# Optimization experiments

Measured on AMD Instinct MI355X. Metric: run time of the kernel, lower is better.

## Reference

```python
import jax, jax.numpy as jnp
import numpy as np

B, S, H = 4, 2048, 512
E, K = 8, 2
DFF = 4 * H


def setup_inputs() -> dict:
    key = jax.random.key(0)
    ks = jax.random.split(key, 6)
    x = jax.random.normal(ks[0], (B, S, H), dtype=jnp.float32)
    gate_W = jax.random.normal(ks[1], (H, E), dtype=jnp.float32) * 0.02
    gate_b = jnp.zeros((E,), dtype=jnp.float32)
    # Stacked expert params; Linear stored as [in, out] so y = x @ W + b
    W1 = jax.random.normal(ks[2], (E, H, DFF), dtype=jnp.float32) * 0.02
    b1 = jnp.zeros((E, DFF), dtype=jnp.float32)
    W2 = jax.random.normal(ks[3], (E, DFF, H), dtype=jnp.float32) * 0.02
    b2 = jnp.zeros((E, H), dtype=jnp.float32)
    return {"x": x, "gate_W": gate_W, "gate_b": gate_b,
            "W1": W1, "b1": b1, "W2": W2, "b2": b2}


def reference(x, gate_W, gate_b, W1, b1, W2, b2):
    bsz, seq, hid = x.shape
    flat = x.reshape(-1, hid)                       # [T, H]
    T = flat.shape[0]
    gate_logits = flat @ gate_W + gate_b            # [T, E]
    topk_vals, topk_idx = jax.lax.top_k(gate_logits, K)   # [T, K]
    topk_w = jax.nn.softmax(topk_vals, axis=-1)      # softmax over selected logits only

    # Scatter top-k weights into a dense per-token combine matrix [T, E];
    # zero weight where a token is not routed -> identical math to masked dispatch.
    combine = jnp.zeros((T, E), dtype=flat.dtype).at[
        jnp.arange(T)[:, None], topk_idx].add(topk_w)

    out_flat = jnp.zeros_like(flat)
    for e in range(E):  # fixed small loop over structurally distinct experts
        h = jax.nn.gelu(flat @ W1[e] + b1[e], approximate=False) @ W2[e] + b2[e]
        out_flat = out_flat + h * combine[:, e:e + 1]
    out = out_flat.reshape(bsz, seq, hid)

    probs = jax.nn.softmax(gate_logits, axis=-1).mean(axis=0)   # [E]
    l_aux = jnp.sum(probs * probs) * E
    expert_counts = jnp.zeros((E,), dtype=jnp.float32).at[
        topk_idx.reshape(-1)].add(1.0)
    return out, l_aux, expert_counts
```

## Files before the change

### kernel.cpp

```cpp
#include <hip/hip_runtime.h>
#include <math.h>

#define TOK 8192
#define HD  512
#define NE  8
#define DFF 2048

typedef __attribute__((ext_vector_type(8))) short bf16x8;
typedef __attribute__((ext_vector_type(4))) float floatx4;

__device__ inline unsigned short f2bf(float f) {
    union { float f; unsigned u; } v; v.f = f;
    unsigned r = v.u + 0x7FFFu + ((v.u >> 16) & 1u);
    return (unsigned short)(r >> 16);
}

__device__ inline float gelu_exact(float v) {
    return 0.5f * v * (1.f + erff(v * 0.70710678118654752f));
}

typedef __attribute__((address_space(1))) const unsigned int glb_u32;
typedef __attribute__((address_space(3))) unsigned int lds_u32;
__device__ __forceinline__ void gload16(const unsigned short* g, unsigned short* l) {
    __builtin_amdgcn_global_load_lds((glb_u32*)g, (lds_u32*)l, 16, 0, 0);
}

__global__ __launch_bounds__(256) void prep_kernel(
    const float* __restrict__ x, const float* __restrict__ gW, const float* __restrict__ gb,
    const float* __restrict__ W1, const float* __restrict__ W2,
    int* __restrict__ seg_count, float* __restrict__ probs_sum,
    int* __restrict__ seg_token, float* __restrict__ seg_w,
    unsigned short* __restrict__ xb,
    unsigned short* __restrict__ W1t, unsigned short* __restrict__ W2t)
{
    __shared__ __align__(16) char shraw[16896];
    int bid = blockIdx.x;
    int tid = threadIdx.x;

    if (bid >= 32) {
        int b = bid - 32;
        float (*tile)[65] = (float(*)[65])shraw;
        int z = b >> 8, rem = b & 255;
        int xq = rem & 31, yq = rem >> 5;
        const float* src; unsigned short* dst; int C, R, cb, rb;
        if (z < NE) {
            src = W1 + (size_t)z * HD * DFF; dst = W1t + (size_t)z * HD * DFF;
            R = HD; C = DFF; cb = xq; rb = yq;
        } else {
            int e = z - NE;
            src = W2 + (size_t)e * DFF * HD; dst = W2t + (size_t)e * DFF * HD;
            R = DFF; C = HD; cb = yq; rb = xq;
        }
        int c0 = cb * 64, r0 = rb * 64;
        int lc = tid & 63, lrw = tid >> 6;
        #pragma unroll
        for (int rr = lrw; rr < 64; rr += 4)
            tile[rr][lc] = src[(size_t)(r0 + rr) * C + c0 + lc];
        __syncthreads();
        #pragma unroll
        for (int cc = lrw; cc < 64; cc += 4)
            dst[(size_t)(c0 + cc) * R + r0 + lc] = f2bf(tile[lc][cc]);
        return;
    }

    float* sW    = (float*)shraw;
    float* psum  = (float*)(shraw + 16384);
    int*   lcount = (int*)(shraw + 16448);
    int*   lbase  = (int*)(shraw + 16512);

    for (int i = tid; i < HD * NE; i += 256) sW[i] = gW[i];
    if (tid < NE) { psum[tid] = 0.f; lcount[tid] = 0; }
    __syncthreads();

    int t = bid * 256 + tid;
    float logit[NE];
    #pragma unroll
    for (int e = 0; e < NE; e++) logit[e] = gb[e];

    const float4* xr4 = reinterpret_cast<const float4*>(x + (size_t)t * HD);
    ushort4* xbw = reinterpret_cast<ushort4*>(xb + (size_t)t * HD);
    for (int j4 = 0; j4 < HD / 4; j4++) {
        float4 xv = xr4[j4];
        int j = j4 * 4;
        ushort4 o; o.x = f2bf(xv.x); o.y = f2bf(xv.y); o.z = f2bf(xv.z); o.w = f2bf(xv.w);
        xbw[j4] = o;
        #pragma unroll
        for (int e = 0; e < NE; e++) {
            logit[e] += xv.x * sW[(j + 0) * NE + e] + xv.y * sW[(j + 1) * NE + e]
                      + xv.z * sW[(j + 2) * NE + e] + xv.w * sW[(j + 3) * NE + e];
        }
    }

    float mx = logit[0];
    #pragma unroll
    for (int e = 1; e < NE; e++) mx = fmaxf(mx, logit[e]);
    float pe[NE]; float s = 0.f;
    #pragma unroll
    for (int e = 0; e < NE; e++) { pe[e] = expf(logit[e] - mx); s += pe[e]; }
    float inv = 1.f / s;
    int l = tid & 63;
    #pragma unroll
    for (int e = 0; e < NE; e++) {
        float v = pe[e] * inv;
        for (int off = 32; off; off >>= 1) v += __shfl_down(v, off);
        if (l == 0) atomicAdd(&psum[e], v);
    }

    int i0 = 0; float v0 = logit[0];
    #pragma unroll
    for (int e = 1; e < NE; e++) if (logit[e] > v0) { v0 = logit[e]; i0 = e; }
    int i1 = -1; float v1 = -3.4e38f;
    #pragma unroll
    for (int e = 0; e < NE; e++) if (e != i0 && logit[e] > v1) { v1 = logit[e]; i1 = e; }
    float e1 = expf(v1 - v0);
    float w0 = 1.f / (1.f + e1);
    float w1 = e1 / (1.f + e1);

    int r0 = atomicAdd(&lcount[i0], 1);
    int r1 = atomicAdd(&lcount[i1], 1);
    __syncthreads();
    if (tid < NE) lbase[tid] = atomicAdd(&seg_count[tid], lcount[tid]);
    __syncthreads();
    int p0 = lbase[i0] + r0;
    seg_token[i0 * TOK + p0] = t;
    seg_w[i0 * TOK + p0] = w0;
    int p1 = lbase[i1] + r1;
    seg_token[i1 * TOK + p1] = t | (1 << 16);
    seg_w[i1 * TOK + p1] = w1;

    __syncthreads();
    if (tid < NE) atomicAdd(&probs_sum[tid], psum[tid]);
}

#define TM  128
#define TN  128
#define BK  32

__global__ __launch_bounds__(256) void gemm1_kernel(
    const unsigned short* __restrict__ xb,
    const unsigned short* __restrict__ W1t,
    const float* __restrict__ bias1,
    const int* __restrict__ seg_count, const float* __restrict__ probs_sum,
    const int* __restrict__ seg_token,
    unsigned short* __restrict__ hbuf,
    float* __restrict__ out_tail)
{
    int bid = blockIdx.x;
    int tid = threadIdx.x;

    if (bid == 0) {
        if (tid < NE) out_tail[1 + tid] = (float)seg_count[tid];
        else if (tid == 64) {
            float s = 0.f;
            #pragma unroll
            for (int e2 = 0; e2 < NE; e2++) {
                float p = probs_sum[e2] * (1.f / (float)TOK);
                s += p * p;
            }
            out_tail[0] = s * (float)NE;
        }
    }

    int e  = bid & 7;
    int r2 = bid >> 3;
    int nb = r2 & 15;
    int mb = r2 >> 4;
    int cnt = seg_count[e];
    if (mb * TM >= cnt) return;
    int off_e = 0;
    #pragma unroll
    for (int ee = 0; ee < NE; ee++) if (ee < e) off_e += (seg_count[ee] + 127) & ~127;
    int hb = off_e + mb * TM;

    __shared__ __align__(16) unsigned short smem[3][2][TM * BK];
    __shared__ int tok_s[TM];
    if (tid < TM) {
        int gi = mb * TM + tid;
        tok_s[tid] = seg_token[e * TOK + ((gi < cnt) ? gi : 0)] & 0xFFFF;
    }
    __syncthreads();

    int w = tid >> 6, l = tid & 63;
    int lr = l & 15, crow = (l >> 4) * 4;
    int wm = (w & 1) * 64, wn = (w >> 1) * 64;
    int rsw = ((l >> 4) ^ ((lr >> 1) & 3)) * 8;
    const unsigned short* w1e = W1t + (size_t)e * DFF * HD + (size_t)(nb * TN) * HD;

    unsigned csrc = (unsigned)(((l & 3) ^ ((l >> 3) & 3)) * 8);
    unsigned aofs[2], bofs[2];
    #pragma unroll
    for (int s = 0; s < 2; s++) {
        int r = w * 32 + s * 16 + (l >> 2);
        aofs[s] = (unsigned)tok_s[r] * HD + csrc;
        bofs[s] = (unsigned)(r * HD) + csrc;
    }

    floatx4 acc[4][4];
    #pragma unroll
    for (int i = 0; i < 4; i++)
        #pragma unroll
        for (int j = 0; j < 4; j++) acc[i][j] = (floatx4){0.f, 0.f, 0.f, 0.f};

    #pragma unroll
    for (int p = 0; p < 2; p++)
        #pragma unroll
        for (int s = 0; s < 2; s++) {
            gload16(xb  + aofs[s] + p * BK, &smem[p][0][(w * 32 + s * 16) * BK]);
            gload16(w1e + bofs[s] + p * BK, &smem[p][1][(w * 32 + s * 16) * BK]);
        }

    const int NIT = HD / BK;
    int rb = 0;
    for (int k = 0; k < NIT; ++k) {
        if (k + 1 < NIT) asm volatile("s_waitcnt vmcnt(4)" ::: "memory");
        else             asm volatile("s_waitcnt vmcnt(0)" ::: "memory");
        __builtin_amdgcn_s_barrier();
        asm volatile("" ::: "memory");
        if (k + 2 < NIT) {
            int ib = (rb == 0) ? 2 : rb - 1;
            int ko = (k + 2) * BK;
            #pragma unroll
            for (int s = 0; s < 2; s++) {
                gload16(xb  + aofs[s] + ko, &smem[ib][0][(w * 32 + s * 16) * BK]);
                gload16(w1e + bofs[s] + ko, &smem[ib][1][(w * 32 + s * 16) * BK]);
            }
        }
        const unsigned short* A = smem[rb][0];
        const unsigned short* B = smem[rb][1];
        bf16x8 a[4], b[4];
        #pragma unroll
        for (int i = 0; i < 4; i++) a[i] = *(const bf16x8*)&A[(wm + 16 * i + lr) * BK + rsw];
        #pragma unroll
        for (int j = 0; j < 4; j++) b[j] = *(const bf16x8*)&B[(wn + 16 * j + lr) * BK + rsw];
        __builtin_amdgcn_s_setprio(1);
        #pragma unroll
        for (int i = 0; i < 4; i++)
            #pragma unroll
            for (int j = 0; j < 4; j++)
                acc[i][j] = __builtin_amdgcn_mfma_f32_16x16x32_bf16(a[i], b[j], acc[i][j], 0, 0, 0);
        __builtin_amdgcn_s_setprio(0);
        rb = (rb == 2) ? 0 : rb + 1;
    }
    __syncthreads();

    unsigned short* scr = &smem[0][0][0] + w * 64 * 72;
    #pragma unroll
    for (int j = 0; j < 4; j++) {
        float b1v = bias1[e * DFF + nb * TN + wn + 16 * j + lr];
        #pragma unroll
        for (int i = 0; i < 4; i++)
            #pragma unroll
            for (int rr = 0; rr < 4; rr++)
                scr[(16 * i + crow + rr) * 72 + 16 * j + lr] = f2bf(gelu_exact(acc[i][j][rr] + b1v));
    }
    __syncthreads();
    int lh = l >> 3, ll = l & 7;
    #pragma unroll
    for (int k = 0; k < 8; k++) {
        uint4 v = *(const uint4*)&scr[(8 * k + lh) * 72 + ll * 8];
        int grow = hb + wm + 8 * k + lh;
        *(uint4*)&hbuf[(size_t)grow * DFF + nb * TN + wn + ll * 8] = v;
    }
}

__global__ __launch_bounds__(256) void gemm2_kernel(
    const unsigned short* __restrict__ hbuf,
    const unsigned short* __restrict__ W2t,
    const float* __restrict__ b2,
    const int* __restrict__ seg_count, const int* __restrict__ seg_token,
    const float* __restrict__ seg_w,
    float* __restrict__ pout,
    float* __restrict__ out,
    int use_pout)
{
    int bid = blockIdx.x;
    int tid = threadIdx.x;
    int e  = bid & 7;
    int r2 = bid >> 3;
    int nb = r2 & 3;
    int mb = r2 >> 2;
    int cnt = seg_count[e];
    if (mb * TM >= cnt) return;
    int off_e = 0;
    #pragma unroll
    for (int ee = 0; ee < NE; ee++) if (ee < e) off_e += (seg_count[ee] + 127) & ~127;
    int hb = off_e + mb * TM;

    __shared__ __align__(16) unsigned short smem[3][2][TM * BK];
    __shared__ int   tok_s[TM];
    __shared__ int   rnk_s[TM];
    __shared__ float wgt_s[TM];
    if (tid < TM) {
        int gi = mb * TM + tid;
        int raw = seg_token[e * TOK + ((gi < cnt) ? gi : 0)];
        tok_s[tid] = raw & 0xFFFF;
        rnk_s[tid] = raw >> 16;
        wgt_s[tid] = (gi < cnt) ? seg_w[e * TOK + gi] : 0.f;
    }
    __syncthreads();

    int w = tid >> 6, l = tid & 63;
    int lr = l & 15, crow = (l >> 4) * 4;
    int wm = (w & 1) * 64, wn = (w >> 1) * 64;
    int rsw = ((l >> 4) ^ ((lr >> 1) & 3)) * 8;
    const unsigned short* w2e = W2t + (size_t)e * HD * DFF + (size_t)(nb * TN) * DFF;

    unsigned csrc = (unsigned)(((l & 3) ^ ((l >> 3) & 3)) * 8);
    unsigned aofs[2], bofs[2];
    #pragma unroll
    for (int s = 0; s < 2; s++) {
        int r = w * 32 + s * 16 + (l >> 2);
        aofs[s] = (unsigned)((hb + r) * DFF) + csrc;
        bofs[s] = (unsigned)(r * DFF) + csrc;
    }

    floatx4 acc[4][4];
    #pragma unroll
    for (int i = 0; i < 4; i++)
        #pragma unroll
        for (int j = 0; j < 4; j++) acc[i][j] = (floatx4){0.f, 0.f, 0.f, 0.f};

    #pragma unroll
    for (int p = 0; p < 2; p++)
        #pragma unroll
        for (int s = 0; s < 2; s++) {
            gload16(hbuf + aofs[s] + p * BK, &smem[p][0][(w * 32 + s * 16) * BK]);
            gload16(w2e  + bofs[s] + p * BK, &smem[p][1][(w * 32 + s * 16) * BK]);
        }

    const int NIT = DFF / BK;
    int rb = 0;
    for (int k = 0; k < NIT; ++k) {
        if (k + 1 < NIT) asm volatile("s_waitcnt vmcnt(4)" ::: "memory");
        else             asm volatile("s_waitcnt vmcnt(0)" ::: "memory");
        __builtin_amdgcn_s_barrier();
        asm volatile("" ::: "memory");
        if (k + 2 < NIT) {
            int ib = (rb == 0) ? 2 : rb - 1;
            int ko = (k + 2) * BK;
            #pragma unroll
            for (int s = 0; s < 2; s++) {
                gload16(hbuf + aofs[s] + ko, &smem[ib][0][(w * 32 + s * 16) * BK]);
                gload16(w2e  + bofs[s] + ko, &smem[ib][1][(w * 32 + s * 16) * BK]);
            }
        }
        const unsigned short* A = smem[rb][0];
        const unsigned short* B = smem[rb][1];
        bf16x8 a[4], b[4];
        #pragma unroll
        for (int i = 0; i < 4; i++) a[i] = *(const bf16x8*)&A[(wm + 16 * i + lr) * BK + rsw];
        #pragma unroll
        for (int j = 0; j < 4; j++) b[j] = *(const bf16x8*)&B[(wn + 16 * j + lr) * BK + rsw];
        __builtin_amdgcn_s_setprio(1);
        #pragma unroll
        for (int i = 0; i < 4; i++)
            #pragma unroll
            for (int j = 0; j < 4; j++)
                acc[i][j] = __builtin_amdgcn_mfma_f32_16x16x32_bf16(a[i], b[j], acc[i][j], 0, 0, 0);
        __builtin_amdgcn_s_setprio(0);
        rb = (rb == 2) ? 0 : rb + 1;
    }

    if (use_pout) {
        #pragma unroll
        for (int j = 0; j < 4; j++) {
            int n = nb * TN + wn + 16 * j + lr;
            float b2v = b2[e * HD + n];
            #pragma unroll
            for (int i = 0; i < 4; i++)
                #pragma unroll
                for (int rr = 0; rr < 4; rr++) {
                    int m = wm + 16 * i + crow + rr;
                    if (mb * TM + m < cnt)
                        pout[((size_t)tok_s[m] * 2 + rnk_s[m]) * HD + n] =
                            (acc[i][j][rr] + b2v) * wgt_s[m];
                }
        }
    } else {
        #pragma unroll
        for (int j = 0; j < 4; j++) {
            int n = nb * TN + wn + 16 * j + lr;
            float b2v = b2[e * HD + n];
            #pragma unroll
            for (int i = 0; i < 4; i++)
                #pragma unroll
                for (int rr = 0; rr < 4; rr++) {
                    int m = wm + 16 * i + crow + rr;
                    atomicAdd(&out[(size_t)tok_s[m] * HD + n], (acc[i][j][rr] + b2v) * wgt_s[m]);
                }
        }
    }
}

__global__ __launch_bounds__(256) void combine_kernel(
    const float* __restrict__ pout, float* __restrict__ out)
{
    int idx = blockIdx.x * 256 + threadIdx.x;
    int t = idx >> 7;
    int c4 = idx & 127;
    const float4* p = (const float4*)pout;
    float4 a = p[((size_t)t * 2 + 0) * 128 + c4];
    float4 b = p[((size_t)t * 2 + 1) * 128 + c4];
    float4 r; r.x = a.x + b.x; r.y = a.y + b.y; r.z = a.z + b.z; r.w = a.w + b.w;
    ((float4*)out)[idx] = r;
}

#define BMT 64
#define FK  64
#define XS_LD 520
#define HS_LD 72

__global__ __launch_bounds__(256, 2) void ffn_fused_fallback(
    const unsigned short* __restrict__ xb,
    const unsigned short* __restrict__ W1t, const float* __restrict__ b1,
    const unsigned short* __restrict__ W2t, const float* __restrict__ b2,
    const int* __restrict__ seg_count, const int* __restrict__ seg_token,
    const float* __restrict__ seg_w, float* __restrict__ out)
{
    int bid = blockIdx.x;
    int e = bid & 7;
    int g = bid >> 3;
    int cnt = seg_count[e];
    int n0 = g * BMT;
    if (n0 >= cnt) return;
    int rows = min(BMT, cnt - n0);

    __shared__ unsigned short xs[BMT * XS_LD];
    __shared__ unsigned short hs[BMT * HS_LD];
    __shared__ int   tok_s[BMT];
    __shared__ float wgt_s[BMT];

    int tid = threadIdx.x;
    if (tid < BMT) {
        int idx = (tid < rows) ? (n0 + tid) : n0;
        tok_s[tid] = seg_token[e * TOK + idx] & 0xFFFF;
        wgt_s[tid] = (tid < rows) ? seg_w[e * TOK + idx] : 0.f;
    }
    __syncthreads();
    {
        int r = tid >> 2, q = tid & 3;
        const uint4* src = (const uint4*)(xb + (size_t)tok_s[r] * HD) + q * 16;
        uint4* dst = (uint4*)&xs[(size_t)r * XS_LD + q * 128];
        #pragma unroll
        for (int i = 0; i < 16; i++) dst[i] = src[i];
    }
    __syncthreads();

    int w = tid >> 6, l = tid & 63;
    int lr = l & 15, lk = (l >> 4) * 8, crow = (l >> 4) * 4;

    const unsigned short* w1e = W1t + (size_t)e * DFF * HD;
    const unsigned short* w2e = W2t + (size_t)e * HD * DFF;

    floatx4 acc2[4][8];
    #pragma unroll
    for (int i = 0; i < 4; i++)
        #pragma unroll
        for (int j = 0; j < 8; j++) acc2[i][j] = (floatx4){0.f, 0.f, 0.f, 0.f};

    for (int fc = 0; fc < DFF; fc += FK) {
        floatx4 acc1[4];
        #pragma unroll
        for (int t = 0; t < 4; t++) acc1[t] = (floatx4){0.f, 0.f, 0.f, 0.f};
        const unsigned short* w1c = w1e + (size_t)fc * HD;
        for (int ks = 0; ks < HD; ks += 32) {
            bf16x8 a = *(const bf16x8*)&xs[(16 * w + lr) * XS_LD + ks + lk];
            #pragma unroll
            for (int t = 0; t < 4; t++) {
                bf16x8 b = *(const bf16x8*)(w1c + (size_t)(16 * t + lr) * HD + ks + lk);
                acc1[t] = __builtin_amdgcn_mfma_f32_16x16x32_bf16(a, b, acc1[t], 0, 0, 0);
            }
        }
        __syncthreads();
        #pragma unroll
        for (int t = 0; t < 4; t++) {
            float b1v = b1[e * DFF + fc + 16 * t + lr];
            #pragma unroll
            for (int r = 0; r < 4; r++)
                hs[(16 * w + crow + r) * HS_LD + 16 * t + lr] = f2bf(gelu_exact(acc1[t][r] + b1v));
        }
        __syncthreads();
        #pragma unroll
        for (int ks = 0; ks < FK; ks += 32) {
            bf16x8 af[4];
            #pragma unroll
            for (int i = 0; i < 4; i++) af[i] = *(const bf16x8*)&hs[(16 * i + lr) * HS_LD + ks + lk];
            #pragma unroll 4
            for (int j = 0; j < 8; j++) {
                bf16x8 b = *(const bf16x8*)(w2e + (size_t)(128 * w + 16 * j + lr) * DFF + fc + ks + lk);
                #pragma unroll
                for (int i = 0; i < 4; i++)
                    acc2[i][j] = __builtin_amdgcn_mfma_f32_16x16x32_bf16(af[i], b, acc2[i][j], 0, 0, 0);
            }
        }
    }
    #pragma unroll
    for (int j = 0; j < 8; j++) {
        int n = 128 * w + 16 * j + lr;
        float b2v = b2[e * HD + n];
        #pragma unroll
        for (int i = 0; i < 4; i++)
            #pragma unroll
            for (int r = 0; r < 4; r++) {
                int m = 16 * i + crow + r;
                atomicAdd(&out[(size_t)tok_s[m] * HD + n], (acc2[i][j][r] + b2v) * wgt_s[m]);
            }
    }
}

__global__ void finalize_kernel(const int* __restrict__ seg_count,
                                const float* __restrict__ probs_sum,
                                float* __restrict__ out_tail)
{
    int tid = threadIdx.x;
    if (tid < NE) out_tail[1 + tid] = (float)seg_count[tid];
    if (tid == 0) {
        float s = 0.f;
        #pragma unroll
        for (int e = 0; e < NE; e++) {
            float p = probs_sum[e] * (1.f / (float)TOK);
            s += p * p;
        }
        out_tail[0] = s * (float)NE;
    }
}

extern "C" void kernel_launch(void* const* d_in, const int* in_sizes, int n_in,
                              void* d_out, int out_size, void* d_ws, size_t ws_size,
                              hipStream_t stream)
{
    const float* x  = (const float*)d_in[0];
    const float* gW = (const float*)d_in[1];
    const float* gb = (const float*)d_in[2];
    const float* W1 = (const float*)d_in[3];
    const float* b1 = (const float*)d_in[4];
    const float* W2 = (const float*)d_in[5];
    const float* b2 = (const float*)d_in[6];
    float* out = (float*)d_out;

    char* ws = (char*)d_ws;
    int*   seg_count = (int*)ws;
    float* probs_sum = (float*)(ws + 32);
    int*   seg_token = (int*)(ws + 4096);
    float* seg_w     = (float*)(ws + 4096 + (size_t)NE * TOK * 4);

    const size_t HBUF_BYTES = (size_t)17408 * DFF * 2;

    const size_t F_POUT = 0xA0000;
    const size_t F_XB   = (1u  << 20);
    const size_t F_W1T  = (9u  << 20);
    const size_t F_W2T  = F_POUT + (size_t)TOK * 2 * HD * 4;
    const size_t F_HBUF = F_W2T + ((size_t)NE * DFF * HD * 2);
    const size_t WS_FAST = F_HBUF + HBUF_BYTES;

    const size_t M_XB   = (1u  << 20);
    const size_t M_W1T  = (16u << 20);
    const size_t M_W2T  = (32u << 20);
    const size_t M_HBUF = (48u << 20);
    const size_t WS_MID = M_HBUF + HBUF_BYTES;

    hipMemsetAsync(d_ws, 0, 64, stream);

    if (ws_size >= WS_FAST) {
        unsigned short* xb   = (unsigned short*)(ws + F_XB);
        unsigned short* W1t  = (unsigned short*)(ws + F_W1T);
        unsigned short* W2t  = (unsigned short*)(ws + F_W2T);
        unsigned short* hbuf = (unsigned short*)(ws + F_HBUF);
        float*          pout = (float*)(ws + F_POUT);

        prep_kernel<<<4128, 256, 0, stream>>>(x, gW, gb, W1, W2,
                                              seg_count, probs_sum, seg_token, seg_w,
                                              xb, W1t, W2t);
        gemm1_kernel<<<NE * (DFF / TN) * 64, 256, 0, stream>>>(
            xb, W1t, b1, seg_count, probs_sum, seg_token, hbuf,
            out + (size_t)TOK * HD);
        gemm2_kernel<<<NE * (HD / TN) * 64, 256, 0, stream>>>(
            hbuf, W2t, b2, seg_count, seg_token, seg_w, pout, out, 1);
        combine_kernel<<<(TOK * HD / 4) / 256, 256, 0, stream>>>(pout, out);
    } else if (ws_size >= WS_MID) {
        unsigned short* xb   = (unsigned short*)(ws + M_XB);
        unsigned short* W1t  = (unsigned short*)(ws + M_W1T);
        unsigned short* W2t  = (unsigned short*)(ws + M_W2T);
        unsigned short* hbuf = (unsigned short*)(ws + M_HBUF);

        hipMemsetAsync(d_out, 0, (size_t)TOK * HD * sizeof(float), stream);
        prep_kernel<<<4128, 256, 0, stream>>>(x, gW, gb, W1, W2,
                                              seg_count, probs_sum, seg_token, seg_w,
                                              xb, W1t, W2t);
        gemm1_kernel<<<NE * (DFF / TN) * 64, 256, 0, stream>>>(
            xb, W1t, b1, seg_count, probs_sum, seg_token, hbuf,
            out + (size_t)TOK * HD);
        gemm2_kernel<<<NE * (HD / TN) * 64, 256, 0, stream>>>(
            hbuf, W2t, b2, seg_count, seg_token, seg_w, (float*)ws, out, 0);
    } else {
        unsigned short* xb   = (unsigned short*)(ws + M_XB);
        unsigned short* W1t  = (unsigned short*)(ws + M_W1T);
        unsigned short* W2t  = (unsigned short*)(ws + M_W2T);

        hipMemsetAsync(d_out, 0, (size_t)TOK * HD * sizeof(float), stream);
        prep_kernel<<<4128, 256, 0, stream>>>(x, gW, gb, W1, W2,
                                              seg_count, probs_sum, seg_token, seg_w,
                                              xb, W1t, W2t);
        finalize_kernel<<<1, 64, 0, stream>>>(seg_count, probs_sum, out + (size_t)TOK * HD);
        ffn_fused_fallback<<<(TOK / BMT) * NE, 256, 0, stream>>>(
            xb, W1t, b1, W2t, b2, seg_count, seg_token, seg_w, out);
    }
}
```

Baseline: 354.8 us.

## Load weight B-fragments directly into registers and vectorize weight transpose

Both expert GEMMs stop staging the weight (B) tiles through LDS. Each wave now loads its MFMA B fragments straight from global memory into registers, double-buffered one K-step ahead, while the gathered activation (A) tiles keep the triple-buffered LDS path. The goal is to halve LDS traffic and footprint per block and remove the LDS reads for B, at the cost of more register use and uncoalesced 16-byte global loads per lane with hand-tuned vmcnt waits. The prologue weight transpose also switches to float4 reads and 16-byte bf16 writes.

```diff
diff --git a/kernel.cpp b/kernel.cpp
--- a/kernel.cpp
+++ b/kernel.cpp
@@ -52,14 +52,24 @@
             R = DFF; C = HD; cb = yq; rb = xq;
         }
         int c0 = cb * 64, r0 = rb * 64;
-        int lc = tid & 63, lrw = tid >> 6;
-        #pragma unroll
-        for (int rr = lrw; rr < 64; rr += 4)
-            tile[rr][lc] = src[(size_t)(r0 + rr) * C + c0 + lc];
+        int tq = (tid & 15) * 4, tr4 = tid >> 4;
+        #pragma unroll
+        for (int p = 0; p < 4; p++) {
+            int rr = tr4 + 16 * p;
+            float4 v = *(const float4*)&src[(size_t)(r0 + rr) * C + c0 + tq];
+            tile[rr][tq + 0] = v.x; tile[rr][tq + 1] = v.y;
+            tile[rr][tq + 2] = v.z; tile[rr][tq + 3] = v.w;
+        }
         __syncthreads();
-        #pragma unroll
-        for (int cc = lrw; cc < 64; cc += 4)
-            dst[(size_t)(c0 + cc) * R + r0 + lc] = f2bf(tile[lc][cc]);
+        int cc = tid >> 3, cq = (tid & 7) * 8;
+        #pragma unroll
+        for (int p = 0; p < 2; p++) {
+            int c = cc + 32 * p;
+            union { unsigned short s[8]; uint4 v; } u8;
+            #pragma unroll
+            for (int u = 0; u < 8; u++) u8.s[u] = f2bf(tile[cq + u][c]);
+            *(uint4*)&dst[(size_t)(c0 + c) * R + r0 + cq] = u8.v;
+        }
         return;
     }
 
@@ -135,6 +145,33 @@
 #define TM  128
 #define TN  128
 #define BK  32
+
+#define GEMM_ITER(KK, BU, BF, W1S, W2S, ISSA, ISSB, SRC_A, SRC_B, LDB) { \
+    asm volatile("s_waitcnt vmcnt(" W1S ")" ::: "memory"); \
+    __builtin_amdgcn_s_barrier(); \
+    asm volatile("" ::: "memory"); \
+    if (ISSA) { int ko = ((KK) + 2) * BK; \
+        gload16(SRC_A + aofs[0] + ko, &smem[rb2][(w * 32) * BK]); \
+        gload16(SRC_A + aofs[1] + ko, &smem[rb2][(w * 32 + 16) * BK]); } \
+    if (ISSB) { int ko = ((KK) + 1) * BK; \
+        _Pragma("unroll") \
+        for (int j = 0; j < 4; j++) { \
+            const unsigned short* bp = SRC_B + (size_t)(wn + 16 * j + lr) * (LDB) + ko + kq; \
+            asm volatile("global_load_dwordx4 %0, %1, off" : "=&v"(BF[j]) : "v"(bp) : "memory"); } } \
+    { const unsigned short* Ab = smem[rb]; \
+      bf16x8 a_[4]; \
+      _Pragma("unroll") \
+      for (int i = 0; i < 4; i++) a_[i] = *(const bf16x8*)&Ab[(wm + 16 * i + lr) * BK + rsw]; \
+      asm volatile("s_waitcnt vmcnt(" W2S ")" ::: "memory"); \
+      __builtin_amdgcn_sched_barrier(0); \
+      __builtin_amdgcn_s_setprio(1); \
+      _Pragma("unroll") \
+      for (int i = 0; i < 4; i++) \
+        _Pragma("unroll") \
+        for (int j = 0; j < 4; j++) \
+            acc[i][j] = __builtin_amdgcn_mfma_f32_16x16x32_bf16(a_[i], BU[j], acc[i][j], 0, 0, 0); \
+      __builtin_amdgcn_s_setprio(0); } \
+    rb = (rb == 2) ? 0 : rb + 1; rb2 = (rb2 == 2) ? 0 : rb2 + 1; }
 
 __global__ __launch_bounds__(256) void gemm1_kernel(
     const unsigned short* __restrict__ xb,
@@ -172,8 +209,10 @@
     for (int ee = 0; ee < NE; ee++) if (ee < e) off_e += (seg_count[ee] + 127) & ~127;
     int hb = off_e + mb * TM;
 
-    __shared__ __align__(16) unsigned short smem[3][2][TM * BK];
+    __shared__ __align__(16) unsigned short sraw[18432];
     __shared__ int tok_s[TM];
+    unsigned short (*smem)[TM * BK] = (unsigned short (*)[TM * BK])sraw;
+
     if (tid < TM) {
         int gi = mb * TM + tid;
         tok_s[tid] = seg_token[e * TOK + ((gi < cnt) ? gi : 0)] & 0xFFFF;
@@ -183,16 +222,16 @@
     int w = tid >> 6, l = tid & 63;
     int lr = l & 15, crow = (l >> 4) * 4;
     int wm = (w & 1) * 64, wn = (w >> 1) * 64;
+    int kq = (l >> 4) * 8;
     int rsw = ((l >> 4) ^ ((lr >> 1) & 3)) * 8;
     const unsigned short* w1e = W1t + (size_t)e * DFF * HD + (size_t)(nb * TN) * HD;
 
     unsigned csrc = (unsigned)(((l & 3) ^ ((l >> 3) & 3)) * 8);
-    unsigned aofs[2], bofs[2];
+    unsigned aofs[2];
     #pragma unroll
     for (int s = 0; s < 2; s++) {
         int r = w * 32 + s * 16 + (l >> 2);
         aofs[s] = (unsigned)tok_s[r] * HD + csrc;
-        bofs[s] = (unsigned)(r * HD) + csrc;
     }
 
     floatx4 acc[4][4];
@@ -201,49 +240,29 @@
         #pragma unroll
         for (int j = 0; j < 4; j++) acc[i][j] = (floatx4){0.f, 0.f, 0.f, 0.f};
 
+    bf16x8 bA[4], bB[4];
     #pragma unroll
     for (int p = 0; p < 2; p++)
         #pragma unroll
-        for (int s = 0; s < 2; s++) {
-            gload16(xb  + aofs[s] + p * BK, &smem[p][0][(w * 32 + s * 16) * BK]);
-            gload16(w1e + bofs[s] + p * BK, &smem[p][1][(w * 32 + s * 16) * BK]);
-        }
+        for (int s = 0; s < 2; s++)
+            gload16(xb + aofs[s] + p * BK, &smem[p][(w * 32 + s * 16) * BK]);
+    #pragma unroll
+    for (int j = 0; j < 4; j++) {
+        const unsigned short* bp = w1e + (size_t)(wn + 16 * j + lr) * HD + kq;
+        asm volatile("global_load_dwordx4 %0, %1, off" : "=&v"(bA[j]) : "v"(bp) : "memory");
+    }
 
     const int NIT = HD / BK;
-    int rb = 0;
-    for (int k = 0; k < NIT; ++k) {
-        if (k + 1 < NIT) asm volatile("s_waitcnt vmcnt(4)" ::: "memory");
-        else             asm volatile("s_waitcnt vmcnt(0)" ::: "memory");
-        __builtin_amdgcn_s_barrier();
-        asm volatile("" ::: "memory");
-        if (k + 2 < NIT) {
-            int ib = (rb == 0) ? 2 : rb - 1;
-            int ko = (k + 2) * BK;
-            #pragma unroll
-            for (int s = 0; s < 2; s++) {
-                gload16(xb  + aofs[s] + ko, &smem[ib][0][(w * 32 + s * 16) * BK]);
-                gload16(w1e + bofs[s] + ko, &smem[ib][1][(w * 32 + s * 16) * BK]);
-            }
-        }
-        const unsigned short* A = smem[rb][0];
-        const unsigned short* B = smem[rb][1];
-        bf16x8 a[4], b[4];
-        #pragma unroll
-        for (int i = 0; i < 4; i++) a[i] = *(const bf16x8*)&A[(wm + 16 * i + lr) * BK + rsw];
-        #pragma unroll
-        for (int j = 0; j < 4; j++) b[j] = *(const bf16x8*)&B[(wn + 16 * j + lr) * BK + rsw];
-        __builtin_amdgcn_s_setprio(1);
-        #pragma unroll
-        for (int i = 0; i < 4; i++)
-            #pragma unroll
-            for (int j = 0; j < 4; j++)
-                acc[i][j] = __builtin_amdgcn_mfma_f32_16x16x32_bf16(a[i], b[j], acc[i][j], 0, 0, 0);
-        __builtin_amdgcn_s_setprio(0);
-        rb = (rb == 2) ? 0 : rb + 1;
-    }
-    __syncthreads();
-
-    unsigned short* scr = &smem[0][0][0] + w * 64 * 72;
+    int rb = 0, rb2 = 2;
+    for (int k2 = 0; k2 + 2 < NIT; k2 += 2) {
+        GEMM_ITER(k2,     bA, bB, "6", "6", 1, 1, xb, w1e, HD);
+        GEMM_ITER(k2 + 1, bB, bA, "6", "6", 1, 1, xb, w1e, HD);
+    }
+    GEMM_ITER(NIT - 2, bA, bB, "6", "4", 0, 1, xb, w1e, HD);
+    GEMM_ITER(NIT - 1, bB, bA, "4", "0", 0, 0, xb, w1e, HD);
+    __syncthreads();
+
+    unsigned short* scr = sraw + w * 64 * 72;
     #pragma unroll
     for (int j = 0; j < 4; j++) {
         float b1v = bias1[e * DFF + nb * TN + wn + 16 * j + lr];
@@ -286,10 +305,12 @@
     for (int ee = 0; ee < NE; ee++) if (ee < e) off_e += (seg_count[ee] + 127) & ~127;
     int hb = off_e + mb * TM;
 
-    __shared__ __align__(16) unsigned short smem[3][2][TM * BK];
+    __shared__ __align__(16) unsigned short sraw[3][TM * BK];
     __shared__ int   tok_s[TM];
     __shared__ int   rnk_s[TM];
     __shared__ float wgt_s[TM];
+    unsigned short (*smem)[TM * BK] = sraw;
+
     if (tid < TM) {
         int gi = mb * TM + tid;
         int raw = seg_token[e * TOK + ((gi < cnt) ? gi : 0)];
@@ -302,16 +323,16 @@
     int w = tid >> 6, l = tid & 63;
     int lr = l & 15, crow = (l >> 4) * 4;
     int wm = (w & 1) * 64, wn = (w >> 1) * 64;
+    int kq = (l >> 4) * 8;
     int rsw = ((l >> 4) ^ ((lr >> 1) & 3)) * 8;
     const unsigned short* w2e = W2t + (size_t)e * HD * DFF + (size_t)(nb * TN) * DFF;
 
     unsigned csrc = (unsigned)(((l & 3) ^ ((l >> 3) & 3)) * 8);
-    unsigned aofs[2], bofs[2];
+    unsigned aofs[2];
     #pragma unroll
     for (int s = 0; s < 2; s++) {
         int r = w * 32 + s * 16 + (l >> 2);
         aofs[s] = (unsigned)((hb + r) * DFF) + csrc;
-        bofs[s] = (unsigned)(r * DFF) + csrc;
     }
 
     floatx4 acc[4][4];
@@ -320,46 +341,26 @@
         #pragma unroll
         for (int j = 0; j < 4; j++) acc[i][j] = (floatx4){0.f, 0.f, 0.f, 0.f};
 
+    bf16x8 bA[4], bB[4];
     #pragma unroll
     for (int p = 0; p < 2; p++)
         #pragma unroll
-        for (int s = 0; s < 2; s++) {
-            gload16(hbuf + aofs[s] + p * BK, &smem[p][0][(w * 32 + s * 16) * BK]);
-            gload16(w2e  + bofs[s] + p * BK, &smem[p][1][(w * 32 + s * 16) * BK]);
-        }
+        for (int s = 0; s < 2; s++)
+            gload16(hbuf + aofs[s] + p * BK, &smem[p][(w * 32 + s * 16) * BK]);
+    #pragma unroll
+    for (int j = 0; j < 4; j++) {
+        const unsigned short* bp = w2e + (size_t)(wn + 16 * j + lr) * DFF + kq;
+        asm volatile("global_load_dwordx4 %0, %1, off" : "=&v"(bA[j]) : "v"(bp) : "memory");
+    }
 
     const int NIT = DFF / BK;
-    int rb = 0;
-    for (int k = 0; k < NIT; ++k) {
-        if (k + 1 < NIT) asm volatile("s_waitcnt vmcnt(4)" ::: "memory");
-        else             asm volatile("s_waitcnt vmcnt(0)" ::: "memory");
-        __builtin_amdgcn_s_barrier();
-        asm volatile("" ::: "memory");
-        if (k + 2 < NIT) {
-            int ib = (rb == 0) ? 2 : rb - 1;
-            int ko = (k + 2) * BK;
-            #pragma unroll
-            for (int s = 0; s < 2; s++) {
-                gload16(hbuf + aofs[s] + ko, &smem[ib][0][(w * 32 + s * 16) * BK]);
-                gload16(w2e  + bofs[s] + ko, &smem[ib][1][(w * 32 + s * 16) * BK]);
-            }
-        }
-        const unsigned short* A = smem[rb][0];
-        const unsigned short* B = smem[rb][1];
-        bf16x8 a[4], b[4];
-        #pragma unroll
-        for (int i = 0; i < 4; i++) a[i] = *(const bf16x8*)&A[(wm + 16 * i + lr) * BK + rsw];
-        #pragma unroll
-        for (int j = 0; j < 4; j++) b[j] = *(const bf16x8*)&B[(wn + 16 * j + lr) * BK + rsw];
-        __builtin_amdgcn_s_setprio(1);
-        #pragma unroll
-        for (int i = 0; i < 4; i++)
-            #pragma unroll
-            for (int j = 0; j < 4; j++)
-                acc[i][j] = __builtin_amdgcn_mfma_f32_16x16x32_bf16(a[i], b[j], acc[i][j], 0, 0, 0);
-        __builtin_amdgcn_s_setprio(0);
-        rb = (rb == 2) ? 0 : rb + 1;
-    }
+    int rb = 0, rb2 = 2;
+    for (int k2 = 0; k2 + 2 < NIT; k2 += 2) {
+        GEMM_ITER(k2,     bA, bB, "6", "6", 1, 1, hbuf, w2e, DFF);
+        GEMM_ITER(k2 + 1, bB, bA, "6", "6", 1, 1, hbuf, w2e, DFF);
+    }
+    GEMM_ITER(NIT - 2, bA, bB, "6", "4", 0, 1, hbuf, w2e, DFF);
+    GEMM_ITER(NIT - 1, bB, bA, "4", "0", 0, 0, hbuf, w2e, DFF);
 
     if (use_pout) {
         #pragma unroll
```

After: 447.5 us. 26.1% more time.
